# Performance work log

Measured on AMD Instinct MI355X. Metric: run time of the kernel, lower is better.

The kernel has to match this reference:

```python
import jax, jax.numpy as jnp
import numpy as np

B, N, IN_DIM, HEADS, PER_HEAD = 8, 512, 256, 4, 32
OUT_DIM = HEADS * PER_HEAD  # 128
NEG_SLOPE = 0.2


def setup_inputs() -> dict:
    key = jax.random.key(0)
    ks = jax.random.split(key, 8)
    x = jax.random.normal(ks[0], (B, N, IN_DIM), jnp.float32)
    adj = jax.random.randint(ks[1], (B, N, N), 0, 2, jnp.int32)
    sl = 1.0 / np.sqrt(IN_DIM)
    W_l = jax.random.normal(ks[2], (IN_DIM, OUT_DIM), jnp.float32) * sl  # source proj
    b_l = jnp.zeros((OUT_DIM,), jnp.float32)
    W_r = jax.random.normal(ks[3], (IN_DIM, OUT_DIM), jnp.float32) * sl  # target proj
    b_r = jnp.zeros((OUT_DIM,), jnp.float32)
    att = jax.random.normal(ks[4], (HEADS, PER_HEAD), jnp.float32) * (1.0 / np.sqrt(PER_HEAD))
    bias = jnp.zeros((OUT_DIM,), jnp.float32)
    return {"x": x, "adj": adj, "W_l": W_l, "b_l": b_l, "W_r": W_r, "b_r": b_r,
            "att": att, "bias": bias}


def _gatv2_single(x_b, adj_b, W_l, b_l, W_r, b_r, att, bias):
    # PyG GATv2Conv: remove_self_loops + add_self_loops -> diagonal forced to 1
    n = x_b.shape[0]
    adj_sl = jnp.fill_diagonal(adj_b, 1, inplace=False)
    # edge_index = adj.nonzero().t(): source = row, target = col
    m = (adj_sl != 0).T  # m[i, j]: source j feeds target i
    xl = (x_b @ W_l + b_l).reshape(n, HEADS, PER_HEAD)  # source-side features
    xr = (x_b @ W_r + b_r).reshape(n, HEADS, PER_HEAD)  # target-side features
    s = xr[:, None] + xl[None, :]                       # [i, j, H, C]
    s = jnp.where(s > 0, s, NEG_SLOPE * s)              # LeakyReLU(0.2)
    e = jnp.einsum('ijhc,hc->ijh', s, att)              # attention logits
    e = jnp.where(m[..., None], e, -jnp.inf)
    alpha = jax.nn.softmax(e, axis=1)                   # softmax over sources j
    out = jnp.einsum('ijh,jhc->ihc', alpha, xl).reshape(n, HEADS * PER_HEAD)
    return out + bias


def reference(x, adj, W_l, b_l, W_r, b_r, att, bias):
    # Sequential per-batch processing, faithful to the original Python loop
    # and keeping the [N,N,H,C] intermediate to one graph at a time.
    def one(args):
        x_b, adj_b = args
        return _gatv2_single(x_b, adj_b, W_l, b_l, W_r, b_r, att, bias)
    return jax.lax.map(one, (x, adj))  # [B, N, OUT_DIM]
```

## Files before the change

### kernel.cpp

```cpp
#include <hip/hip_runtime.h>
#include <hip/hip_bf16.h>

#define B_   8
#define N_   512
#define IND  256
#define H_   4
#define PH   32
#define OD   128
#define TI   4

typedef float v2f __attribute__((ext_vector_type(2)));

#define ATT_SCALE 0.5770780163555854f
#define DLR_SCALE 0.8656170245333781f

template <int PAT>
__device__ __forceinline__ float dpp_add(float x) {
    int yi = __builtin_amdgcn_mov_dpp(__float_as_int(x), PAT, 0xF, 0xF, true);
    return x + __int_as_float(yi);
}

__device__ __forceinline__ float fast_exp2(float x) {
#if __has_builtin(__builtin_amdgcn_exp2f)
    return __builtin_amdgcn_exp2f(x);
#else
    return exp2f(x);
#endif
}

__device__ __forceinline__ void pk_fma(v2f& d, v2f a, v2f b) {
    asm("v_pk_fma_f32 %0, %1, %2, %0" : "+v"(d) : "v"(a), "v"(b));
}
__device__ __forceinline__ v2f pk_add(v2f a, v2f b) {
    v2f d;
    asm("v_pk_add_f32 %0, %1, %2" : "=v"(d) : "v"(a), "v"(b));
    return d;
}

__global__ __launch_bounds__(256) void pack_kernel(
    const int* __restrict__ adj, unsigned char* __restrict__ packT)
{
    const int t = threadIdx.x;
    const int lane = t & 63;
    const int r = blockIdx.x * 4 + (t >> 6);
    const int j = r & (N_ - 1);
    const int b = r >> 9;
    const int* row = adj + (size_t)r * N_;
    #pragma unroll
    for (int k = 0; k < 8; ++k) {
        const int i = k * 64 + lane;
        int a = row[i];
        unsigned long long m = __ballot(a != 0 || i == j);
        if (lane < 16) {
            const int iq = k * 16 + lane;
            packT[((size_t)(b * 128 + iq)) * N_ + j] =
                (unsigned char)((m >> (lane * 4)) & 15ull);
        }
    }
}

__global__ __launch_bounds__(256, 2) void proj_kernel(
    const float* __restrict__ x,
    const float* __restrict__ Wl, const float* __restrict__ bl,
    const float* __restrict__ Wr, const float* __restrict__ br,
    const float* __restrict__ att,
    float* __restrict__ xl, float* __restrict__ xr,
    float* __restrict__ dlT, float* __restrict__ drT)
{
    __shared__ float xs[8 * IND];
    const int t = threadIdx.x;
    const int row0 = blockIdx.x * 8;

    const float4* xp4 = (const float4*)(x + (size_t)row0 * IND);
    float4* xs4 = (float4*)xs;
    #pragma unroll
    for (int k = 0; k < 2; ++k)
        xs4[t + k * 256] = xp4[t + k * 256];
    __syncthreads();

    const int which = t >> 7;
    const int rg = (t >> 6) & 1;
    const int og = t & 63;
    const int o0 = og * 2;
    const int r0 = rg * 4;
    const float* W  = which ? Wr : Wl;
    const float* bb = which ? br : bl;

    float acc0[4], acc1[4];
    #pragma unroll
    for (int r = 0; r < 4; ++r) { acc0[r] = 0.f; acc1[r] = 0.f; }

    for (int k = 0; k < IND; k += 4) {
        float wf0[4], wf1[4];
        #pragma unroll
        for (int kk = 0; kk < 4; ++kk) {
            float2 wv = *(const float2*)(W + (size_t)(k + kk) * OD + o0);
            wf0[kk] = wv.x;
            wf1[kk] = wv.y;
        }
        float xv[4][4];
        #pragma unroll
        for (int r = 0; r < 4; ++r)
            *(float4*)(xv[r]) = *(const float4*)(&xs[(r0 + r) * IND + k]);
        #pragma unroll
        for (int kk = 0; kk < 4; ++kk)
            #pragma unroll
            for (int r = 0; r < 4; ++r) {
                acc0[r] = fmaf(xv[r][kk], wf0[kk], acc0[r]);
                acc1[r] = fmaf(xv[r][kk], wf1[kk], acc1[r]);
            }
    }

    const float bv0 = bb[o0];
    const float bv1 = bb[o0 + 1];
    const float a0 = att[o0];
    const float a1 = att[o0 + 1];
    float* dst = which ? xr : xl;
    float* dp  = which ? drT : dlT;
    float dcon[4];
    #pragma unroll
    for (int r = 0; r < 4; ++r) {
        float y0 = acc0[r] + bv0;
        float y1 = acc1[r] + bv1;
        *(float2*)(&dst[(size_t)(row0 + r0 + r) * OD + o0]) = make_float2(y0, y1);
        dcon[r] = fmaf(a0, y0, a1 * y1);
    }
    #pragma unroll
    for (int m = 1; m < 16; m <<= 1) {
        #pragma unroll
        for (int r = 0; r < 4; ++r)
            dcon[r] += __shfl_xor(dcon[r], m);
    }
    if ((og & 15) == 0) {
        const int h = og >> 4;
        #pragma unroll
        for (int r = 0; r < 4; ++r) {
            const int n = row0 + r0 + r;
            const int bb2 = n >> 9, nn = n & (N_ - 1);
            dp[((size_t)(bb2 * H_ + h)) * N_ + nn] = DLR_SCALE * dcon[r];
        }
    }
}

__global__ __launch_bounds__(256, 3) void attn_kernel(
    const unsigned char* __restrict__ packT,
    const float* __restrict__ att,
    const float* __restrict__ xl, const float* __restrict__ xr,
    const float* __restrict__ dlT, const float* __restrict__ drT,
    float* __restrict__ pacc, float* __restrict__ psum)
{
    const int t = threadIdx.x;
    const int s   = blockIdx.x & 1;
    const int blk = blockIdx.x >> 1;
    const int b  = blk >> 7;
    const int i0 = (blk & 127) * TI;
    const int cq = t & 3;
    const int js = (t >> 2) & 15;
    const int h  = t >> 6;
    const int cbase = h * PH + cq * 8;
    const int j0 = s * 256;

    float atS[8];
    {
        const float* ap = att + cbase;
        float4 a0 = *(const float4*)(ap);
        float4 a1 = *(const float4*)(ap + 4);
        atS[0] = ATT_SCALE * a0.x; atS[1] = ATT_SCALE * a0.y;
        atS[2] = ATT_SCALE * a0.z; atS[3] = ATT_SCALE * a0.w;
        atS[4] = ATT_SCALE * a1.x; atS[5] = ATT_SCALE * a1.y;
        atS[6] = ATT_SCALE * a1.z; atS[7] = ATT_SCALE * a1.w;
    }
    v2f xr2[TI][4];
    float drv[TI];
    #pragma unroll
    for (int il = 0; il < TI; ++il) {
        const float* xp = xr + ((size_t)(b * N_ + i0 + il)) * OD + cbase;
        float4 r0 = *(const float4*)(xp);
        float4 r1 = *(const float4*)(xp + 4);
        xr2[il][0] = (v2f){r0.x, r0.y};
        xr2[il][1] = (v2f){r0.z, r0.w};
        xr2[il][2] = (v2f){r1.x, r1.y};
        xr2[il][3] = (v2f){r1.z, r1.w};
        drv[il] = drT[((size_t)(b * H_ + h)) * N_ + i0 + il];
    }

    v2f acc[TI][4];
    float sumw[TI];
    #pragma unroll
    for (int il = 0; il < TI; ++il) {
        sumw[il] = 0.f;
        #pragma unroll
        for (int m = 0; m < 4; ++m) acc[il][m] = (v2f){0.f, 0.f};
    }

    const float*         xlp = xl + ((size_t)(b * N_ + j0 + js)) * OD + cbase;
    const unsigned char* ptp = packT + ((size_t)(b * 128 + (i0 >> 2))) * N_ + j0 + js;
    const float*         dlp = dlT + ((size_t)(b * H_ + h)) * N_ + j0 + js;

    float4   va = *(const float4*)(xlp);
    float4   vb = *(const float4*)(xlp + 4);
    unsigned pj = *ptp;
    float    dj = *dlp;

    #pragma unroll 2
    for (int u = 0; u < 16; ++u) {
        float4   wa = va, wb = vb;
        unsigned wp = pj;
        float    wd = dj;
        if (u < 15) {
            xlp += 16 * OD; ptp += 16; dlp += 16;
            va = *(const float4*)(xlp);
            vb = *(const float4*)(xlp + 4);
            pj = *ptp;
            dj = *dlp;
        }
        v2f p0 = (v2f){wa.x, wa.y}, p1 = (v2f){wa.z, wa.w};
        v2f p2 = (v2f){wb.x, wb.y}, p3 = (v2f){wb.z, wb.w};
        #pragma unroll
        for (int il = 0; il < TI; ++il) {
            float e2a = 0.f, e2b = 0.f;
            v2f sv;
            sv = pk_add(xr2[il][0], p0);
            e2a = fmaf(atS[0], __builtin_fabsf(sv.x), e2a);
            e2b = fmaf(atS[1], __builtin_fabsf(sv.y), e2b);
            sv = pk_add(xr2[il][1], p1);
            e2a = fmaf(atS[2], __builtin_fabsf(sv.x), e2a);
            e2b = fmaf(atS[3], __builtin_fabsf(sv.y), e2b);
            sv = pk_add(xr2[il][2], p2);
            e2a = fmaf(atS[4], __builtin_fabsf(sv.x), e2a);
            e2b = fmaf(atS[5], __builtin_fabsf(sv.y), e2b);
            sv = pk_add(xr2[il][3], p3);
            e2a = fmaf(atS[6], __builtin_fabsf(sv.x), e2a);
            e2b = fmaf(atS[7], __builtin_fabsf(sv.y), e2b);
            float eh = e2a + e2b;
            eh = dpp_add<0xB1>(eh);
            eh = dpp_add<0x4E>(eh);
            float e = (wd + drv[il]) + eh;
            float ex = fast_exp2(e);
            float w = (wp & (1u << il)) ? ex : 0.f;
            sumw[il] += w;
            v2f ws = (v2f){w, w};
            pk_fma(acc[il][0], ws, p0);
            pk_fma(acc[il][1], ws, p1);
            pk_fma(acc[il][2], ws, p2);
            pk_fma(acc[il][3], ws, p3);
        }
    }

    #pragma unroll
    for (int il = 0; il < TI; ++il) {
        sumw[il] += __shfl_xor(sumw[il], 4);
        sumw[il] += __shfl_xor(sumw[il], 8);
        sumw[il] += __shfl_xor(sumw[il], 16);
        sumw[il] += __shfl_xor(sumw[il], 32);
    }

    float accf[32];
    #pragma unroll
    for (int il = 0; il < TI; ++il)
        #pragma unroll
        for (int m = 0; m < 4; ++m) {
            accf[il * 8 + 2 * m]     = acc[il][m].x;
            accf[il * 8 + 2 * m + 1] = acc[il][m].y;
        }

    float r16[16];
    {
        const bool hi = (js & 1) != 0;
        #pragma unroll
        for (int m = 0; m < 16; ++m) {
            float send = hi ? accf[m] : accf[16 + m];
            float keep = hi ? accf[16 + m] : accf[m];
            r16[m] = keep + __shfl_xor(send, 4);
        }
    }
    float r8[8];
    {
        const bool hi = (js & 2) != 0;
        #pragma unroll
        for (int m = 0; m < 8; ++m) {
            float send = hi ? r16[m] : r16[8 + m];
            float keep = hi ? r16[8 + m] : r16[m];
            r8[m] = keep + __shfl_xor(send, 8);
        }
    }
    float r4[4];
    {
        const bool hi = (js & 4) != 0;
        #pragma unroll
        for (int m = 0; m < 4; ++m) {
            float send = hi ? r8[m] : r8[4 + m];
            float keep = hi ? r8[4 + m] : r8[m];
            r4[m] = keep + __shfl_xor(send, 16);
        }
    }
    float r2[2];
    {
        const bool hi = (js & 8) != 0;
        #pragma unroll
        for (int m = 0; m < 2; ++m) {
            float send = hi ? r4[m] : r4[2 + m];
            float keep = hi ? r4[2 + m] : r4[m];
            r2[m] = keep + __shfl_xor(send, 32);
        }
    }

    const int il = ((js & 1) << 1) | ((js >> 1) & 1);
    const int coff = ((js >> 2) & 1) * 4 + ((js >> 3) & 1) * 2;
    const int c = cbase + coff;
    float* pa = pacc + (size_t)s * (B_ * N_ * OD)
                     + ((size_t)(b * N_ + i0 + il)) * OD + c;
    *(float2*)pa = make_float2(r2[0], r2[1]);
    if ((t & 63) == 0) {
        float* ps = psum + s * (B_ * N_ * H_);
        #pragma unroll
        for (int q = 0; q < TI; ++q)
            ps[(size_t)(b * N_ + i0 + q) * H_ + h] = sumw[q];
    }
}

__global__ __launch_bounds__(256) void combine_kernel(
    const float* __restrict__ pacc, const float* __restrict__ psum,
    const float* __restrict__ bias, float* __restrict__ out)
{
    const int idx = blockIdx.x * 256 + threadIdx.x;
    const int n = idx >> 6;
    const int c = (idx & 63) * 2;
    const int h = c >> 5;
    float2 a0 = *(const float2*)(pacc + (size_t)n * OD + c);
    float2 a1 = *(const float2*)(pacc + (size_t)B_ * N_ * OD + (size_t)n * OD + c);
    float sden = psum[(size_t)n * H_ + h] + psum[B_ * N_ * H_ + (size_t)n * H_ + h];
    float inv = 1.f / sden;
    *(float2*)(out + (size_t)n * OD + c) =
        make_float2(fmaf(a0.x + a1.x, inv, bias[c]),
                    fmaf(a0.y + a1.y, inv, bias[c + 1]));
}

extern "C" void kernel_launch(void* const* d_in, const int* in_sizes, int n_in,
                              void* d_out, int out_size, void* d_ws, size_t ws_size,
                              hipStream_t stream) {
    const float* x    = (const float*)d_in[0];
    const int*   adj  = (const int*)d_in[1];
    const float* Wl   = (const float*)d_in[2];
    const float* bl   = (const float*)d_in[3];
    const float* Wr   = (const float*)d_in[4];
    const float* br   = (const float*)d_in[5];
    const float* att  = (const float*)d_in[6];
    const float* bias = (const float*)d_in[7];
    float* out = (float*)d_out;

    float* ws = (float*)d_ws;
    float* xl   = ws;
    float* xr   = xl + (size_t)B_ * N_ * OD;
    float* dlT  = xr + (size_t)B_ * N_ * OD;
    float* drT  = dlT + (size_t)B_ * N_ * H_;
    float* pacc = drT + (size_t)B_ * N_ * H_;
    float* psum = pacc + (size_t)2 * B_ * N_ * OD;
    unsigned char* packT =
        (unsigned char*)(psum + (size_t)2 * B_ * N_ * H_);

    pack_kernel<<<1024, 256, 0, stream>>>(adj, packT);
    proj_kernel<<<512, 256, 0, stream>>>(x, Wl, bl, Wr, br, att, xl, xr, dlT, drT);
    attn_kernel<<<2048, 256, 0, stream>>>(packT, att, xl, xr, dlT, drT, pacc, psum);
    combine_kernel<<<1024, 256, 0, stream>>>(pacc, psum, bias, out);
}
```

Measured before the change: 132.2 us.

## Remove source split and fuse combine into attention kernel

The attention kernel no longer splits the 512 source nodes across two blocks. Each block now walks all 32 source chunks with a two-deep register prefetch, then normalizes by the softmax sum and adds bias directly into the output. This removes the combine kernel launch and the partial accumulator and sum round-trip through global memory. In exchange, the grid shrinks from 2048 to 1024 blocks, which lowers parallelism and latency hiding, and the extra prefetch registers may raise register pressure.

```diff
diff --git a/kernel.cpp b/kernel.cpp
--- a/kernel.cpp
+++ b/kernel.cpp
@@ -144,21 +144,18 @@
 
 __global__ __launch_bounds__(256, 3) void attn_kernel(
     const unsigned char* __restrict__ packT,
-    const float* __restrict__ att,
+    const float* __restrict__ att, const float* __restrict__ bias,
     const float* __restrict__ xl, const float* __restrict__ xr,
     const float* __restrict__ dlT, const float* __restrict__ drT,
-    float* __restrict__ pacc, float* __restrict__ psum)
+    float* __restrict__ out)
 {
     const int t = threadIdx.x;
-    const int s   = blockIdx.x & 1;
-    const int blk = blockIdx.x >> 1;
-    const int b  = blk >> 7;
-    const int i0 = (blk & 127) * TI;
+    const int b  = blockIdx.x >> 7;
+    const int i0 = (blockIdx.x & 127) * TI;
     const int cq = t & 3;
     const int js = (t >> 2) & 15;
     const int h  = t >> 6;
     const int cbase = h * PH + cq * 8;
-    const int j0 = s * 256;
 
     float atS[8];
     {
@@ -193,26 +190,32 @@
         for (int m = 0; m < 4; ++m) acc[il][m] = (v2f){0.f, 0.f};
     }
 
-    const float*         xlp = xl + ((size_t)(b * N_ + j0 + js)) * OD + cbase;
-    const unsigned char* ptp = packT + ((size_t)(b * 128 + (i0 >> 2))) * N_ + j0 + js;
-    const float*         dlp = dlT + ((size_t)(b * H_ + h)) * N_ + j0 + js;
-
-    float4   va = *(const float4*)(xlp);
-    float4   vb = *(const float4*)(xlp + 4);
-    unsigned pj = *ptp;
-    float    dj = *dlp;
+    const float*         xlp = xl + ((size_t)(b * N_ + js)) * OD + cbase;
+    const unsigned char* ptp = packT + ((size_t)(b * 128 + (i0 >> 2))) * N_ + js;
+    const float*         dlp = dlT + ((size_t)(b * H_ + h)) * N_ + js;
+
+    float4   va0 = *(const float4*)(xlp);
+    float4   vb0 = *(const float4*)(xlp + 4);
+    unsigned pj0 = *ptp;
+    float    dj0 = *dlp;
+    xlp += 16 * OD; ptp += 16; dlp += 16;
+    float4   va1 = *(const float4*)(xlp);
+    float4   vb1 = *(const float4*)(xlp + 4);
+    unsigned pj1 = *ptp;
+    float    dj1 = *dlp;
 
     #pragma unroll 2
-    for (int u = 0; u < 16; ++u) {
-        float4   wa = va, wb = vb;
-        unsigned wp = pj;
-        float    wd = dj;
-        if (u < 15) {
+    for (int u = 0; u < 32; ++u) {
+        float4   wa = va0, wb = vb0;
+        unsigned wp = pj0;
+        float    wd = dj0;
+        va0 = va1; vb0 = vb1; pj0 = pj1; dj0 = dj1;
+        if (u < 30) {
             xlp += 16 * OD; ptp += 16; dlp += 16;
-            va = *(const float4*)(xlp);
-            vb = *(const float4*)(xlp + 4);
-            pj = *ptp;
-            dj = *dlp;
+            va1 = *(const float4*)(xlp);
+            vb1 = *(const float4*)(xlp + 4);
+            pj1 = *ptp;
+            dj1 = *dlp;
         }
         v2f p0 = (v2f){wa.x, wa.y}, p1 = (v2f){wa.z, wa.w};
         v2f p2 = (v2f){wb.x, wb.y}, p3 = (v2f){wb.z, wb.w};
@@ -308,32 +311,12 @@
     const int il = ((js & 1) << 1) | ((js >> 1) & 1);
     const int coff = ((js >> 2) & 1) * 4 + ((js >> 3) & 1) * 2;
     const int c = cbase + coff;
-    float* pa = pacc + (size_t)s * (B_ * N_ * OD)
-                     + ((size_t)(b * N_ + i0 + il)) * OD + c;
-    *(float2*)pa = make_float2(r2[0], r2[1]);
-    if ((t & 63) == 0) {
-        float* ps = psum + s * (B_ * N_ * H_);
-        #pragma unroll
-        for (int q = 0; q < TI; ++q)
-            ps[(size_t)(b * N_ + i0 + q) * H_ + h] = sumw[q];
-    }
-}
-
-__global__ __launch_bounds__(256) void combine_kernel(
-    const float* __restrict__ pacc, const float* __restrict__ psum,
-    const float* __restrict__ bias, float* __restrict__ out)
-{
-    const int idx = blockIdx.x * 256 + threadIdx.x;
-    const int n = idx >> 6;
-    const int c = (idx & 63) * 2;
-    const int h = c >> 5;
-    float2 a0 = *(const float2*)(pacc + (size_t)n * OD + c);
-    float2 a1 = *(const float2*)(pacc + (size_t)B_ * N_ * OD + (size_t)n * OD + c);
-    float sden = psum[(size_t)n * H_ + h] + psum[B_ * N_ * H_ + (size_t)n * H_ + h];
-    float inv = 1.f / sden;
-    *(float2*)(out + (size_t)n * OD + c) =
-        make_float2(fmaf(a0.x + a1.x, inv, bias[c]),
-                    fmaf(a0.y + a1.y, inv, bias[c + 1]));
+    const float sw0 = (js & 1) ? ((js & 2) ? sumw[3] : sumw[2])
+                               : ((js & 2) ? sumw[1] : sumw[0]);
+    const float inv = 1.f / sw0;
+    float* op = out + ((size_t)(b * N_ + i0 + il)) * OD;
+    *(float2*)(&op[c]) = make_float2(fmaf(r2[0], inv, bias[c]),
+                                     fmaf(r2[1], inv, bias[c + 1]));
 }
 
 extern "C" void kernel_launch(void* const* d_in, const int* in_sizes, int n_in,
@@ -350,17 +333,14 @@
     float* out = (float*)d_out;
 
     float* ws = (float*)d_ws;
-    float* xl   = ws;
-    float* xr   = xl + (size_t)B_ * N_ * OD;
-    float* dlT  = xr + (size_t)B_ * N_ * OD;
-    float* drT  = dlT + (size_t)B_ * N_ * H_;
-    float* pacc = drT + (size_t)B_ * N_ * H_;
-    float* psum = pacc + (size_t)2 * B_ * N_ * OD;
+    float* xl  = ws;
+    float* xr  = xl + (size_t)B_ * N_ * OD;
+    float* dlT = xr + (size_t)B_ * N_ * OD;
+    float* drT = dlT + (size_t)B_ * N_ * H_;
     unsigned char* packT =
-        (unsigned char*)(psum + (size_t)2 * B_ * N_ * H_);
+        (unsigned char*)(drT + (size_t)B_ * N_ * H_);
 
     pack_kernel<<<1024, 256, 0, stream>>>(adj, packT);
     proj_kernel<<<512, 256, 0, stream>>>(x, Wl, bl, Wr, br, att, xl, xr, dlT, drT);
-    attn_kernel<<<2048, 256, 0, stream>>>(packT, att, xl, xr, dlT, drT, pacc, psum);
-    combine_kernel<<<1024, 256, 0, stream>>>(pacc, psum, bias, out);
-}
+    attn_kernel<<<1024, 256, 0, stream>>>(packT, att, bias, xl, xr, dlT, drT, out);
+}
```

New measurement: 130.6 us. About the same (-1.2%).
